# Optimization experiments

Measured on AMD Instinct MI355X. Metric: run time of the kernel, lower is better.

Reference implementation:

```python
import jax, jax.numpy as jnp
import numpy as np

IN_DIM = 256
OUT_DIM = 256

def setup_inputs() -> dict:
    key = jax.random.key(0)
    k1, k2, k3, k4 = jax.random.split(key, 4)
    B, N, K, D = 4, 10000, 16, IN_DIM
    x = jax.random.normal(k1, (B, N, D), dtype=jnp.float32)
    neigh = jax.random.randint(k2, (N, K), 0, N, dtype=jnp.int64)
    # nn.Linear(2*in_dim, out_dim): W [out, 2*in], b [out]
    bound = 1.0 / np.sqrt(2 * D)
    W = jax.random.uniform(k3, (OUT_DIM, 2 * D), minval=-bound, maxval=bound, dtype=jnp.float32)
    b = jax.random.uniform(k4, (OUT_DIM,), minval=-bound, maxval=bound, dtype=jnp.float32)
    return {"x": x, "neigh": neigh, "W": W, "b": b}

def reference(x, neigh, W, b):
    # x: [B,N,D], neigh: [N,K] with -1 = padding
    mask = (neigh >= 0)                                # [N,K]
    idx = jnp.clip(neigh, 0, None)                     # [N,K]
    # batch_gather_nodes: x_nei[b,n,k,:] = x[b, idx[n,k], :]
    x_nei = x[:, idx, :]                               # [B,N,K,D]
    x_nei = x_nei * mask[None, :, :, None].astype(x.dtype)
    denom = jnp.clip(mask.sum(axis=1), 1, None).astype(x.dtype)  # [N]
    agg = x_nei.sum(axis=2) / denom[None, :, None]     # [B,N,D]
    h = jnp.concatenate([x, agg], axis=-1)             # [B,N,2D]
    return jax.nn.relu(jnp.einsum('bnd,od->bno', h, W) + b)
```

## Files before the change

### kernel.cpp

```cpp
#include <hip/hip_runtime.h>
#include <hip/hip_bf16.h>
#include <stdint.h>

#define B_   4
#define N_   10000
#define K_   16
#define D_   256
#define OUT_ 256
#define KDIM 512
#define M_   (B_ * N_)
#define CW   32
#define NCH  8
#define CHUNK_ELEMS ((size_t)N_ * B_ * CW)

typedef __attribute__((ext_vector_type(8))) short          short8;
typedef __attribute__((ext_vector_type(8))) unsigned short ushort8;
typedef __attribute__((ext_vector_type(4))) float          f32x4;
typedef __attribute__((ext_vector_type(4))) unsigned short ushort4_t;

__device__ inline unsigned short f2bf(float f) {
    __hip_bfloat16 h = __float2bfloat16(f);
    return *reinterpret_cast<unsigned short*>(&h);
}
__device__ inline float bf2f(unsigned short u) {
    unsigned int v = ((unsigned int)u) << 16;
    return __builtin_bit_cast(float, v);
}

__global__ __launch_bounds__(256) void prep(const float* __restrict__ x,
                                            const float* __restrict__ W,
                                            unsigned short* __restrict__ xc,
                                            unsigned short* __restrict__ Wb) {
    const int t = threadIdx.x;
    if (blockIdx.x < 5000) {
        const int n  = blockIdx.x * 2 + (t >> 7);
        const int b  = (t >> 5) & 3;
        const int c0 = (t & 31) * 8;
        const float4* xr = (const float4*)(x + ((size_t)b * N_ + n) * D_ + c0);
        float4 v0 = xr[0];
        float4 v1 = xr[1];
        ushort8 s;
        s[0] = f2bf(v0.x); s[1] = f2bf(v0.y); s[2] = f2bf(v0.z); s[3] = f2bf(v0.w);
        s[4] = f2bf(v1.x); s[5] = f2bf(v1.y); s[6] = f2bf(v1.z); s[7] = f2bf(v1.w);
        const int ch  = c0 >> 5;
        const int col = c0 & 31;
        *(ushort8*)(xc + (size_t)ch * CHUNK_ELEMS + ((size_t)n * B_ + b) * CW + col) = s;
    } else {
        int g = (blockIdx.x - 5000) * 256 + t;
        float4 v = ((const float4*)W)[g];
        ushort4_t s;
        s.x = f2bf(v.x); s.y = f2bf(v.y); s.z = f2bf(v.z); s.w = f2bf(v.w);
        ((ushort4_t*)Wb)[g] = s;
    }
}

__global__ __launch_bounds__(256) void gather_agg2(const unsigned short* __restrict__ xc,
                                                   const int*            __restrict__ neigh,
                                                   unsigned short*       __restrict__ hagg) {
    const int c   = blockIdx.x & 7;
    const int g   = blockIdx.x >> 3;
    const int n0  = g * 16;
    const int tid = threadIdx.x;

    __shared__ int   idx_s[16 * K_];
    __shared__ float inv_s[16];

    idx_s[tid] = neigh[n0 * K_ + tid];
    __syncthreads();
    if (tid < 16) {
        int cnt = 0;
#pragma unroll
        for (int k = 0; k < K_; ++k) cnt += idx_s[tid * K_ + k] >= 0 ? 1 : 0;
        inv_s[tid] = 1.0f / (float)(cnt > 1 ? cnt : 1);
    }
    __syncthreads();

    const int q  = tid & 3;
    const int tl = tid >> 2;
    const int ns = tl >> 2;
    const int b  = tl & 3;

    const unsigned short* xcc = xc + (size_t)c * CHUNK_ELEMS;

    int jj[K_];
#pragma unroll
    for (int k = 0; k < K_; ++k) jj[k] = idx_s[ns * K_ + k];

    ushort8 vv[K_];
#pragma unroll
    for (int k = 0; k < K_; ++k) {
        const int jc = jj[k] >= 0 ? jj[k] : 0;
        vv[k] = *(const ushort8*)(xcc + ((size_t)jc * B_ + b) * CW + q * 8);
    }

    float acc[8] = {0.f, 0.f, 0.f, 0.f, 0.f, 0.f, 0.f, 0.f};
#pragma unroll
    for (int k = 0; k < K_; ++k) {
        const float m = jj[k] >= 0 ? 1.f : 0.f;
#pragma unroll
        for (int e = 0; e < 8; ++e) acc[e] += bf2f(vv[k][e]) * m;
    }
    const float inv = inv_s[ns];

    ushort8 s;
#pragma unroll
    for (int e = 0; e < 8; ++e) s[e] = f2bf(acc[e] * inv);
    *(ushort8*)(hagg + ((size_t)b * N_ + n0 + ns) * D_ + c * CW + q * 8) = s;
}

__global__ __launch_bounds__(256) void gemm_bt3(const unsigned short* __restrict__ xc,
                                                const unsigned short* __restrict__ hagg,
                                                const unsigned short* __restrict__ Bm,
                                                const float* __restrict__ bias,
                                                float* __restrict__ out) {
    __shared__ unsigned short As[64 * 32];
    __shared__ unsigned short Bs[256 * 32];

    const int tid    = threadIdx.x;
    const int w      = tid >> 6;
    const int lane   = tid & 63;
    const int tile_m = blockIdx.x * 64;
    const int q      = lane >> 4;
    const int r16    = lane & 15;

    const int crow = lane >> 2;
    const int kofs = (lane & 3) * 8;

    const unsigned short* ps[4];
    const unsigned short* pa[4];
#pragma unroll
    for (int c = 0; c < 4; ++c) {
        const int m  = tile_m + c * 16 + crow;
        const int b  = (m >= N_) + (m >= 2 * N_) + (m >= 3 * N_);
        const int n  = m - b * N_;
        ps[c] = xc + ((size_t)n * B_ + b) * CW + kofs;
        pa[c] = hagg + (size_t)m * D_ + kofs;
    }

    f32x4 acc[4][4] = {};

    for (int kk = 0; kk < KDIM; kk += 32) {
        const int kidx = kk >> 5;
#pragma unroll
        for (int t = 0; t < 5; ++t) {
            const int c = w * 5 + t;
            if (c < 4) {
                const unsigned short* ga = (kk < D_)
                    ? ps[c] + (size_t)kidx * CHUNK_ELEMS
                    : pa[c] + (kk - D_);
                __builtin_amdgcn_global_load_lds(
                    (const __attribute__((address_space(1))) void*)ga,
                    (__attribute__((address_space(3))) void*)(As + c * 512),
                    16, 0, 0);
            } else {
                const int row = (c - 4) * 16 + crow;
                const unsigned short* gb = Bm + (size_t)row * KDIM + kk + kofs;
                __builtin_amdgcn_global_load_lds(
                    (const __attribute__((address_space(1))) void*)gb,
                    (__attribute__((address_space(3))) void*)(Bs + (c - 4) * 512),
                    16, 0, 0);
            }
        }
        __syncthreads();

        short8 a[4], bf[4];
#pragma unroll
        for (int i = 0; i < 4; ++i)
            a[i] = *(const short8*)(As + (i * 16 + r16) * 32 + q * 8);
#pragma unroll
        for (int j = 0; j < 4; ++j)
            bf[j] = *(const short8*)(Bs + (w * 64 + j * 16 + r16) * 32 + q * 8);

#pragma unroll
        for (int i = 0; i < 4; ++i)
#pragma unroll
            for (int j = 0; j < 4; ++j)
                acc[i][j] = __builtin_amdgcn_mfma_f32_16x16x32_bf16(a[i], bf[j], acc[i][j], 0, 0, 0);

        __syncthreads();
    }

    float bj[4];
#pragma unroll
    for (int j = 0; j < 4; ++j)
        bj[j] = bias[w * 64 + j * 16 + r16];

#pragma unroll
    for (int i = 0; i < 4; ++i) {
#pragma unroll
        for (int reg = 0; reg < 4; ++reg) {
            const int m = tile_m + i * 16 + q * 4 + reg;
            float* orow = out + (size_t)m * OUT_ + w * 64;
#pragma unroll
            for (int j = 0; j < 4; ++j) {
                float v = acc[i][j][reg] + bj[j];
                orow[j * 16 + r16] = v > 0.f ? v : 0.f;
            }
        }
    }
}

extern "C" void kernel_launch(void* const* d_in, const int* in_sizes, int n_in,
                              void* d_out, int out_size, void* d_ws, size_t ws_size,
                              hipStream_t stream) {
    const float* x     = (const float*)d_in[0];
    const int*   neigh = (const int*)d_in[1];
    const float* W     = (const float*)d_in[2];
    const float* bias  = (const float*)d_in[3];
    float*       out   = (float*)d_out;

    unsigned short* Wb   = (unsigned short*)d_ws;
    unsigned short* xc   = Wb + OUT_ * KDIM;
    unsigned short* hagg = xc + NCH * CHUNK_ELEMS;

    prep<<<5000 + 128, 256, 0, stream>>>(x, W, xc, Wb);
    gather_agg2<<<(N_ / 16) * NCH, 256, 0, stream>>>(xc, neigh, hagg);
    gemm_bt3<<<M_ / 64, 256, 0, stream>>>(xc, hagg, Wb, bias, out);
}
```

Before: 132.1 us.

## Fuse prep, gather and GEMM into one cooperative persistent kernel

Replaces three kernel launches with a single cooperative kernel of 640 blocks that loops over the prep, gather-aggregate and GEMM work, separated by grid-wide syncs. The goal is to remove launch gaps and tail effects between stages. It also computes the neighbor count per thread instead of in a separate shared-memory pass. In exchange, the GEMM phase runs on only 625 blocks, grid syncs add overhead, and the launch-bounds occupancy hint of 3 may limit registers. The old three-kernel path remains as a fallback if the cooperative launch fails.

```diff
diff --git a/kernel.cpp b/kernel.cpp
--- a/kernel.cpp
+++ b/kernel.cpp
@@ -1,6 +1,9 @@
 #include <hip/hip_runtime.h>
+#include <hip/hip_cooperative_groups.h>
 #include <hip/hip_bf16.h>
 #include <stdint.h>
+
+namespace cg = cooperative_groups;
 
 #define B_   4
 #define N_   10000
@@ -11,6 +14,7 @@
 #define M_   (B_ * N_)
 #define CW   32
 #define NCH  8
+#define GRID 640
 #define CHUNK_ELEMS ((size_t)N_ * B_ * CW)
 
 typedef __attribute__((ext_vector_type(8))) short          short8;
@@ -25,6 +29,177 @@
 __device__ inline float bf2f(unsigned short u) {
     unsigned int v = ((unsigned int)u) << 16;
     return __builtin_bit_cast(float, v);
+}
+
+__global__ __launch_bounds__(256, 3) void mega(const float* __restrict__ x,
+                                               const float* __restrict__ W,
+                                               const int*   __restrict__ neigh,
+                                               const float* __restrict__ bias,
+                                               float*       __restrict__ out,
+                                               unsigned short* __restrict__ xc,
+                                               unsigned short* __restrict__ hagg,
+                                               unsigned short* __restrict__ Wb) {
+    cg::grid_group gg = cg::this_grid();
+    const int tid = threadIdx.x;
+    const int bid = blockIdx.x;
+
+    __shared__ unsigned short As[64 * 32];
+    __shared__ unsigned short Bs[256 * 32];
+    __shared__ int idx_s[256];
+
+    for (int u = bid; u < 5128; u += GRID) {
+        if (u < 5000) {
+            const int n  = u * 2 + (tid >> 7);
+            const int b  = (tid >> 5) & 3;
+            const int c0 = (tid & 31) * 8;
+            const float4* xr = (const float4*)(x + ((size_t)b * N_ + n) * D_ + c0);
+            float4 v0 = xr[0];
+            float4 v1 = xr[1];
+            ushort8 s;
+            s[0] = f2bf(v0.x); s[1] = f2bf(v0.y); s[2] = f2bf(v0.z); s[3] = f2bf(v0.w);
+            s[4] = f2bf(v1.x); s[5] = f2bf(v1.y); s[6] = f2bf(v1.z); s[7] = f2bf(v1.w);
+            const int ch  = c0 >> 5;
+            const int col = c0 & 31;
+            *(ushort8*)(xc + (size_t)ch * CHUNK_ELEMS + ((size_t)n * B_ + b) * CW + col) = s;
+        } else {
+            const int g = (u - 5000) * 256 + tid;
+            float4 v = ((const float4*)W)[g];
+            ushort4_t s;
+            s.x = f2bf(v.x); s.y = f2bf(v.y); s.z = f2bf(v.z); s.w = f2bf(v.w);
+            ((ushort4_t*)Wb)[g] = s;
+        }
+    }
+    __threadfence();
+    gg.sync();
+
+    for (int u = bid; u < 5000; u += GRID) {
+        __syncthreads();
+        idx_s[tid] = neigh[(u >> 3) * 256 + tid];
+        __syncthreads();
+
+        const int c  = u & 7;
+        const int n0 = (u >> 3) * 16;
+        const int q  = tid & 3;
+        const int tl = tid >> 2;
+        const int ns = tl >> 2;
+        const int b  = tl & 3;
+
+        const unsigned short* xcc = xc + (size_t)c * CHUNK_ELEMS;
+
+        int jj[K_];
+        int cnt = 0;
+#pragma unroll
+        for (int k = 0; k < K_; ++k) {
+            jj[k] = idx_s[ns * K_ + k];
+            cnt += jj[k] >= 0 ? 1 : 0;
+        }
+
+        ushort8 vv[K_];
+#pragma unroll
+        for (int k = 0; k < K_; ++k) {
+            const int jc = jj[k] >= 0 ? jj[k] : 0;
+            vv[k] = *(const ushort8*)(xcc + ((size_t)jc * B_ + b) * CW + q * 8);
+        }
+
+        float acc[8] = {0.f, 0.f, 0.f, 0.f, 0.f, 0.f, 0.f, 0.f};
+#pragma unroll
+        for (int k = 0; k < K_; ++k) {
+            const float m = jj[k] >= 0 ? 1.f : 0.f;
+#pragma unroll
+            for (int e = 0; e < 8; ++e) acc[e] += bf2f(vv[k][e]) * m;
+        }
+        const float inv = 1.0f / (float)(cnt > 1 ? cnt : 1);
+
+        ushort8 s;
+#pragma unroll
+        for (int e = 0; e < 8; ++e) s[e] = f2bf(acc[e] * inv);
+        *(ushort8*)(hagg + ((size_t)b * N_ + n0 + ns) * D_ + c * CW + q * 8) = s;
+    }
+    __threadfence();
+    gg.sync();
+
+    if (bid < 625) {
+        const int w      = tid >> 6;
+        const int lane   = tid & 63;
+        const int tile_m = bid * 64;
+        const int q      = lane >> 4;
+        const int r16    = lane & 15;
+        const int crow   = lane >> 2;
+        const int kofs   = (lane & 3) * 8;
+
+        const unsigned short* ps[4];
+        const unsigned short* pa[4];
+#pragma unroll
+        for (int c = 0; c < 4; ++c) {
+            const int m  = tile_m + c * 16 + crow;
+            const int b  = (m >= N_) + (m >= 2 * N_) + (m >= 3 * N_);
+            const int n  = m - b * N_;
+            ps[c] = xc + ((size_t)n * B_ + b) * CW + kofs;
+            pa[c] = hagg + (size_t)m * D_ + kofs;
+        }
+
+        f32x4 acc[4][4] = {};
+
+        for (int kk = 0; kk < KDIM; kk += 32) {
+            const int kidx = kk >> 5;
+#pragma unroll
+            for (int t = 0; t < 5; ++t) {
+                const int c = w * 5 + t;
+                if (c < 4) {
+                    const unsigned short* ga = (kk < D_)
+                        ? ps[c] + (size_t)kidx * CHUNK_ELEMS
+                        : pa[c] + (kk - D_);
+                    __builtin_amdgcn_global_load_lds(
+                        (const __attribute__((address_space(1))) void*)ga,
+                        (__attribute__((address_space(3))) void*)(As + c * 512),
+                        16, 0, 0);
+                } else {
+                    const int row = (c - 4) * 16 + crow;
+                    const unsigned short* gb = Wb + (size_t)row * KDIM + kk + kofs;
+                    __builtin_amdgcn_global_load_lds(
+                        (const __attribute__((address_space(1))) void*)gb,
+                        (__attribute__((address_space(3))) void*)(Bs + (c - 4) * 512),
+                        16, 0, 0);
+                }
+            }
+            __syncthreads();
+
+            short8 a[4], bf[4];
+#pragma unroll
+            for (int i = 0; i < 4; ++i)
+                a[i] = *(const short8*)(As + (i * 16 + r16) * 32 + q * 8);
+#pragma unroll
+            for (int j = 0; j < 4; ++j)
+                bf[j] = *(const short8*)(Bs + (w * 64 + j * 16 + r16) * 32 + q * 8);
+
+#pragma unroll
+            for (int i = 0; i < 4; ++i)
+#pragma unroll
+                for (int j = 0; j < 4; ++j)
+                    acc[i][j] = __builtin_amdgcn_mfma_f32_16x16x32_bf16(a[i], bf[j], acc[i][j], 0, 0, 0);
+
+            __syncthreads();
+        }
+
+        float bj[4];
+#pragma unroll
+        for (int j = 0; j < 4; ++j)
+            bj[j] = bias[w * 64 + j * 16 + r16];
+
+#pragma unroll
+        for (int i = 0; i < 4; ++i) {
+#pragma unroll
+            for (int reg = 0; reg < 4; ++reg) {
+                const int m = tile_m + i * 16 + q * 4 + reg;
+                float* orow = out + (size_t)m * OUT_ + w * 64;
+#pragma unroll
+                for (int j = 0; j < 4; ++j) {
+                    float v = acc[i][j][reg] + bj[j];
+                    orow[j * 16 + r16] = v > 0.f ? v : 0.f;
+                }
+            }
+        }
+    }
 }
 
 __global__ __launch_bounds__(256) void prep(const float* __restrict__ x,
@@ -62,17 +237,8 @@
     const int n0  = g * 16;
     const int tid = threadIdx.x;
 
-    __shared__ int   idx_s[16 * K_];
-    __shared__ float inv_s[16];
-
+    __shared__ int idx_s[16 * K_];
     idx_s[tid] = neigh[n0 * K_ + tid];
-    __syncthreads();
-    if (tid < 16) {
-        int cnt = 0;
-#pragma unroll
-        for (int k = 0; k < K_; ++k) cnt += idx_s[tid * K_ + k] >= 0 ? 1 : 0;
-        inv_s[tid] = 1.0f / (float)(cnt > 1 ? cnt : 1);
-    }
     __syncthreads();
 
     const int q  = tid & 3;
@@ -83,8 +249,12 @@
     const unsigned short* xcc = xc + (size_t)c * CHUNK_ELEMS;
 
     int jj[K_];
-#pragma unroll
-    for (int k = 0; k < K_; ++k) jj[k] = idx_s[ns * K_ + k];
+    int cnt = 0;
+#pragma unroll
+    for (int k = 0; k < K_; ++k) {
+        jj[k] = idx_s[ns * K_ + k];
+        cnt += jj[k] >= 0 ? 1 : 0;
+    }
 
     ushort8 vv[K_];
 #pragma unroll
@@ -100,7 +270,7 @@
 #pragma unroll
         for (int e = 0; e < 8; ++e) acc[e] += bf2f(vv[k][e]) * m;
     }
-    const float inv = inv_s[ns];
+    const float inv = 1.0f / (float)(cnt > 1 ? cnt : 1);
 
     ushort8 s;
 #pragma unroll
@@ -122,9 +292,8 @@
     const int tile_m = blockIdx.x * 64;
     const int q      = lane >> 4;
     const int r16    = lane & 15;
-
-    const int crow = lane >> 2;
-    const int kofs = (lane & 3) * 8;
+    const int crow   = lane >> 2;
+    const int kofs   = (lane & 3) * 8;
 
     const unsigned short* ps[4];
     const unsigned short* pa[4];
@@ -213,7 +382,14 @@
     unsigned short* xc   = Wb + OUT_ * KDIM;
     unsigned short* hagg = xc + NCH * CHUNK_ELEMS;
 
-    prep<<<5000 + 128, 256, 0, stream>>>(x, W, xc, Wb);
-    gather_agg2<<<(N_ / 16) * NCH, 256, 0, stream>>>(xc, neigh, hagg);
-    gemm_bt3<<<M_ / 64, 256, 0, stream>>>(xc, hagg, Wb, bias, out);
-}
+    void* args[] = { (void*)&x, (void*)&W, (void*)&neigh, (void*)&bias,
+                     (void*)&out, (void*)&xc, (void*)&hagg, (void*)&Wb };
+    hipError_t err = hipLaunchCooperativeKernel((const void*)mega,
+                                                dim3(GRID), dim3(256),
+                                                args, 0, stream);
+    if (err != hipSuccess) {
+        prep<<<5000 + 128, 256, 0, stream>>>(x, W, xc, Wb);
+        gather_agg2<<<(N_ / 16) * NCH, 256, 0, stream>>>(xc, neigh, hagg);
+        gemm_bt3<<<M_ / 64, 256, 0, stream>>>(xc, hagg, Wb, bias, out);
+    }
+}
```

Measured after the change: 442.3 us. +234.8%, slower.
